# Performance work log

Hardware: AMD Instinct MI355X
Metric: run time of the kernel (lower is better)

Reference implementation:

```python
import jax, jax.numpy as jnp
import numpy as np

DIM = 128
EXPAND = 2
INTERNAL = DIM * EXPAND  # 256
MAX_SEQ = 2048
BATCH = 32
GATE_DECAY = 3.0


def _gated_cell(x, Wa, ba, Wi, bi, g):
    # x: [B,S,D]; Wa,Wi: [E,D]; ba,bi,g: [E]
    pa = jnp.einsum('bsd,ed->bse', x, Wa) + ba          # projected activation
    pi = jnp.einsum('bsd,ed->bse', x, Wi) + bi          # projected input
    reset_gate = jax.nn.sigmoid(pa)
    input_gate = jax.nn.sigmoid(pi)
    alpha = jax.nn.sigmoid(g)                           # [E]
    a = alpha / jnp.power(GATE_DECAY, reset_gate)       # adaptive alpha [B,S,E]
    u = jnp.sqrt(1.0 - a * a) * (input_gate * pi)       # per-step input [B,S,E]

    def step(h, au):
        a_t, u_t = au
        h = a_t * h + u_t
        return h, h

    h0 = jnp.zeros((x.shape[0], Wa.shape[0]), x.dtype)
    _, ys = jax.lax.scan(step, h0, (a.transpose(1, 0, 2), u.transpose(1, 0, 2)))
    return ys.transpose(1, 0, 2)                        # [B,S,E]


def _recency_weights(seq_len, dtype):
    w = jnp.exp(jnp.linspace(0.0, 3.0, MAX_SEQ))[:seq_len]
    return w.astype(dtype).reshape(1, -1, 1)


def setup_inputs() -> dict:
    key = jax.random.key(0)
    ks = jax.random.split(key, 12)
    std = 1.0 / np.sqrt(DIM)  # kaiming fan_in linear
    lo = float(np.log(0.9 / 0.1))
    hi = float(np.log(0.999 / 0.001))
    d = {
        'x': jax.random.normal(ks[0], (BATCH, MAX_SEQ, DIM), jnp.float32),
        'Wa_u': jax.random.normal(ks[1], (INTERNAL, DIM), jnp.float32) * std,
        'ba_u': jnp.zeros((INTERNAL,), jnp.float32),
        'Wi_u': jax.random.normal(ks[2], (INTERNAL, DIM), jnp.float32) * std,
        'bi_u': jnp.zeros((INTERNAL,), jnp.float32),
        'g_u': jax.random.uniform(ks[3], (INTERNAL,), jnp.float32, lo, hi),
        'Wa_w': jax.random.normal(ks[4], (INTERNAL, DIM), jnp.float32) * std,
        'ba_w': jnp.zeros((INTERNAL,), jnp.float32),
        'Wi_w': jax.random.normal(ks[5], (INTERNAL, DIM), jnp.float32) * std,
        'bi_w': jnp.zeros((INTERNAL,), jnp.float32),
        'g_w': jax.random.uniform(ks[6], (INTERNAL,), jnp.float32, lo, hi),
        'Wf': jax.random.normal(ks[7], (DIM, 4 * DIM), jnp.float32) * (1.0 / np.sqrt(4 * DIM)),
        'bf': jnp.zeros((DIM,), jnp.float32),
    }
    return d


def reference(x, Wa_u, ba_u, Wi_u, bi_u, g_u, Wa_w, ba_w, Wi_w, bi_w, g_w, Wf, bf):
    unweighted = _gated_cell(x, Wa_u, ba_u, Wi_u, bi_u, g_u)          # [B,S,2D]
    xw = x * _recency_weights(x.shape[1], x.dtype)
    weighted = _gated_cell(xw, Wa_w, ba_w, Wi_w, bi_w, g_w)           # [B,S,2D]
    combined = jnp.concatenate([unweighted, weighted], axis=-1)       # [B,S,4D]
    return jnp.einsum('bsf,df->bsd', combined, Wf) + bf               # [B,S,D]
```

## Files before the change

### kernel.cpp

```cpp
#include <hip/hip_runtime.h>
#include <hip/hip_fp16.h>
#include <cstddef>
#include <cstdint>

#define DIM 128
#define SEQ 2048
#define NB 32
#define NCH 512
#define NROWS (NB * SEQ)

typedef _Float16 half8 __attribute__((ext_vector_type(8)));
typedef float    f32x4 __attribute__((ext_vector_type(4)));

#define CMB_BYTES ((size_t)NROWS * NCH * 2)
#define WFG_OFF   CMB_BYTES
#define WFG_BYTES ((size_t)NCH * DIM * 2)
#define WS_NEEDED (WFG_OFF + WFG_BYTES)

__device__ __forceinline__ float sigf(float v) {
    return __builtin_amdgcn_rcpf(1.0f + __builtin_amdgcn_exp2f(v * -1.44269504f));
}

__device__ __forceinline__ half8 cvt8(float4 v0, float4 v1) {
    auto p0 = __builtin_amdgcn_cvt_pkrtz(v0.x, v0.y);
    auto p1 = __builtin_amdgcn_cvt_pkrtz(v0.z, v0.w);
    auto p2 = __builtin_amdgcn_cvt_pkrtz(v1.x, v1.y);
    auto p3 = __builtin_amdgcn_cvt_pkrtz(v1.z, v1.w);
    union U { half8 h8; decltype(p0) p[4]; } u;
    u.p[0] = p0; u.p[1] = p1; u.p[2] = p2; u.p[3] = p3;
    return u.h8;
}

__device__ __forceinline__ void gload_lds16(const _Float16* g, _Float16* l) {
    __builtin_amdgcn_global_load_lds(
        (const __attribute__((address_space(1))) void*)g,
        (__attribute__((address_space(3))) void*)l,
        16, 0, 0);
}

__global__ __launch_bounds__(512, 2) void kfused(
        const float* __restrict__ x,
        const float* __restrict__ Wa_u, const float* __restrict__ ba_u,
        const float* __restrict__ Wi_u, const float* __restrict__ bi_u,
        const float* __restrict__ g_u,
        const float* __restrict__ Wa_w, const float* __restrict__ ba_w,
        const float* __restrict__ Wi_w, const float* __restrict__ bi_w,
        const float* __restrict__ g_w,
        const float* __restrict__ Wf, _Float16* __restrict__ Wfg,
        _Float16* __restrict__ cmb) {
    __shared__ _Float16 Bs[8192];
    __shared__ float2   Wseg[2][8][33];
    __shared__ float    carryL[2][32];

    const int tid  = threadIdx.x;
    const int lane = tid & 63;
    const int w    = tid >> 6;
    const int quad = lane >> 4;
    const int n16  = lane & 15;

    const int b  = blockIdx.x;
    const int cg = blockIdx.y;
    const int p  = cg >> 3;
    const int ebase = (cg & 7) * 32;

    if (b == 0) {
        int tg = cg * 512 + tid;
#pragma unroll
        for (int i = 0; i < 8; ++i) {
            int o = tg * 8 + i;
            int j    = o & 7;
            int l2   = (o >> 3) & 63;
            int q2   = l2 >> 4, m16 = l2 & 15;
            int ct   = (o >> 9) & 7;
            int ks2  = (o >> 12) & 1;
            int kb2  = o >> 13;
            int k = kb2 * 64 + ks2 * 32 + q2 * 8 + j;
            int n = ct * 16 + m16;
            Wfg[o] = (_Float16)Wf[n * NCH + k];
        }
    }

    const float* Wa  = p ? Wa_w : Wa_u;
    const float* Wi  = p ? Wi_w : Wi_u;
    const float* bap = p ? ba_w : ba_u;
    const float* bip = p ? bi_w : bi_u;
    const float* gp  = p ? g_w  : g_u;

    for (int sl = tid; sl < 1024; sl += 512) {
        int l  = sl & 63;
        int nt = (sl >> 6) & 3;
        int ks = sl >> 8;
        int qq = l >> 4, nn = l & 15;
        int e = ebase + (nt & 1) * 16 + nn;
        const float* Wp = (nt >> 1) ? Wi : Wa;
        const float* src = Wp + (size_t)e * DIM + ks * 32 + qq * 8;
        float4 v0 = *(const float4*)src;
        float4 v1 = *(const float4*)(src + 4);
        *(half8*)&Bs[sl * 8] = cvt8(v0, v1);
    }

    const float NL2E = -1.44269504f;
    float rba[2], rbi[2], ral[2], rba2[2];
#pragma unroll
    for (int hh = 0; hh < 2; ++hh) {
        int e = ebase + hh * 16 + n16;
        rba[hh] = bap[e];
        rbi[hh] = bip[e];
        ral[hh] = sigf(gp[e]);
        rba2[hh] = rba[hh] * NL2E;
    }
    if (tid < 32) carryL[0][tid] = 0.0f;

    float scb = __expf((float)(w * 16 + quad * 4) * (3.0f / 2047.0f));
    const float r1    = __expf(3.0f / 2047.0f);
    const float r2    = r1 * r1;
    const float r3    = r2 * r1;
    const float cs128 = __expf(128.0f * 3.0f / 2047.0f);

    const float* xbase = x + ((size_t)b * SEQ + (size_t)(w * 16 + n16)) * DIM + quad * 8;
    _Float16* dst0 = cmb + (size_t)(cg >> 1) * 8192 + (size_t)w * 1024
                   + (size_t)(cg & 1) * 512
                   + (size_t)quad * 32 + (size_t)(n16 >> 3) * 128 + (n16 & 7);

    __syncthreads();

    half8 bfr[8];
#pragma unroll
    for (int ks = 0; ks < 2; ++ks)
#pragma unroll
        for (int nt = 0; nt < 4; ++nt)
            bfr[ks * 4 + nt] = *(const half8*)&Bs[(ks * 256 + nt * 64 + lane) * 8];

    half8 af[4];
    {
        float4 xf0[8];
#pragma unroll
        for (int ks = 0; ks < 4; ++ks) {
            xf0[2 * ks]     = *(const float4*)(xbase + ks * 32);
            xf0[2 * ks + 1] = *(const float4*)(xbase + ks * 32 + 4);
        }
#pragma unroll
        for (int ks = 0; ks < 4; ++ks)
            af[ks] = cvt8(xf0[2 * ks], xf0[2 * ks + 1]);
    }

    for (int t = 0; t < 16; ++t) {
        f32x4 acc[4];
#pragma unroll
        for (int nt = 0; nt < 4; ++nt) acc[nt] = (f32x4){0.f, 0.f, 0.f, 0.f};
#pragma unroll
        for (int ks = 0; ks < 4; ++ks) {
            half8 a = af[ks];
#pragma unroll
            for (int nt = 0; nt < 4; ++nt) {
                half8 bb = (ks < 2)
                    ? bfr[ks * 4 + nt]
                    : *(const half8*)&Bs[(ks * 256 + nt * 64 + lane) * 8];
                acc[nt] = __builtin_amdgcn_mfma_f32_16x16x32_f16(a, bb, acc[nt], 0, 0, 0);
            }
        }

        const float* ab = xbase + (size_t)((t + 1) & 15) * 128 * DIM;
        float4 xf1[4];
#pragma unroll
        for (int ks = 0; ks < 2; ++ks) {
            xf1[2 * ks]     = *(const float4*)(ab + ks * 32);
            xf1[2 * ks + 1] = *(const float4*)(ab + ks * 32 + 4);
        }

        float sc[4], sc2[4];
        if (p) { sc[0] = scb; sc[1] = scb * r1; sc[2] = scb * r2; sc[3] = scb * r3; }
        else   { sc[0] = sc[1] = sc[2] = sc[3] = 1.0f; }
        scb *= cs128;
#pragma unroll
        for (int reg = 0; reg < 4; ++reg) sc2[reg] = sc[reg] * NL2E;

        float a_s[2][4], u_s[2][4];
        float IA[2], IU[2], EA[2], EU[2];
#pragma unroll
        for (int hh = 0; hh < 2; ++hh) {
            float A4 = 1.0f, U4 = 0.0f;
#pragma unroll
            for (int reg = 0; reg < 4; ++reg) {
                float pi  = fmaf(acc[2 + hh][reg], sc[reg], rbi[hh]);
                float ea  = __builtin_amdgcn_exp2f(fmaf(acc[hh][reg], sc2[reg], rba2[hh]));
                float rst = __builtin_amdgcn_rcpf(1.0f + ea);
                float ig  = sigf(pi);
                float a   = ral[hh] * __builtin_amdgcn_exp2f(-rst * 1.5849625007211562f);
                float m   = fmaxf(fmaf(-a, a, 1.0f), 0.0f);
                float u   = __builtin_amdgcn_sqrtf(m) * (ig * pi);
                a_s[hh][reg] = a; u_s[hh][reg] = u;
                A4 *= a;
                U4 = fmaf(a, U4, u);
            }
            float A = A4, U = U4;
            float Ap = __shfl_up(A, 16); float Up = __shfl_up(U, 16);
            bool c1 = quad >= 1;
            U = c1 ? fmaf(A, Up, U) : U;
            A = c1 ? A * Ap : A;
            Ap = __shfl_up(A, 32); Up = __shfl_up(U, 32);
            bool c2 = quad >= 2;
            U = c2 ? fmaf(A, Up, U) : U;
            A = c2 ? A * Ap : A;
            IA[hh] = A; IU[hh] = U;
            float Ae = __shfl_up(A, 16), Ue = __shfl_up(U, 16);
            EA[hh] = (quad == 0) ? 1.0f : Ae;
            EU[hh] = (quad == 0) ? 0.0f : Ue;
        }
        if (quad == 3) {
#pragma unroll
            for (int hh = 0; hh < 2; ++hh)
                Wseg[t & 1][w][hh * 16 + n16] = make_float2(IA[hh], IU[hh]);
        }

        __syncthreads();

        float4 xf2[4];
#pragma unroll
        for (int ks = 0; ks < 2; ++ks) {
            xf2[2 * ks]     = *(const float4*)(ab + 64 + ks * 32);
            xf2[2 * ks + 1] = *(const float4*)(ab + 64 + ks * 32 + 4);
        }
        af[0] = cvt8(xf1[0], xf1[1]);
        af[1] = cvt8(xf1[2], xf1[3]);

        _Float16* dstT = dst0 + (size_t)((b * 16 + t) * 8) * 8192;
#pragma unroll
        for (int hh = 0; hh < 2; ++hh) {
            int ch = hh * 16 + n16;
            float h = carryL[t & 1][ch];
            float2 wv[7];
#pragma unroll
            for (int jj = 0; jj < 7; ++jj)
                wv[jj] = Wseg[t & 1][jj][ch];
#pragma unroll
            for (int jj = 0; jj < 7; ++jj)
                if (jj < w) h = fmaf(wv[jj].x, h, wv[jj].y);
            h = fmaf(EA[hh], h, EU[hh]);
#pragma unroll
            for (int reg = 0; reg < 4; ++reg) {
                h = fmaf(a_s[hh][reg], h, u_s[hh][reg]);
                dstT[hh * 256 + reg * 8] = (_Float16)h;
            }
            if (w == 7 && quad == 3)
                carryL[(t + 1) & 1][ch] = h;
        }

        af[2] = cvt8(xf2[0], xf2[1]);
        af[3] = cvt8(xf2[2], xf2[3]);
    }
}

__global__ __launch_bounds__(256, 4) void k3_mfma(
        const _Float16* __restrict__ cmbF, const _Float16* __restrict__ Wfg,
        const float* __restrict__ bfv, float* __restrict__ out) {
    __shared__ _Float16 As[2][4096];

    const int tid  = threadIdx.x;
    const int lane = tid & 63;
    const int w    = tid >> 6;
    const int id   = blockIdx.x;
    const int rb   = id >> 1;
    const int half = id & 1;
    const int rt7  = half * 4 + w;
    const int q    = lane >> 4;
    const int nn   = lane & 15;

    f32x4 acc[8];
#pragma unroll
    for (int ct = 0; ct < 8; ++ct) acc[ct] = (f32x4){0.0f, 0.0f, 0.0f, 0.0f};

#define K3_STAGE(buf, kb)                                                     \
    {                                                                         \
        const _Float16* sa = cmbF + ((size_t)rb * 8 + (kb)) * 8192            \
                           + (size_t)rt7 * 1024 + (size_t)lane * 8;           \
        _Float16* la = &As[buf][w * 1024];                                    \
        gload_lds16(sa, la);                                                  \
        gload_lds16(sa + 512, la + 512);                                      \
    }

    K3_STAGE(0, 0);
    __syncthreads();

    for (int kb = 0; kb < 8; ++kb) {
        const int cur = kb & 1;
        if (kb < 7) K3_STAGE(cur ^ 1, kb + 1);

        const _Float16* bsrc = Wfg + (size_t)kb * 8192 + (size_t)lane * 8;
#pragma unroll
        for (int ks = 0; ks < 2; ++ks) {
            half8 a = *(const half8*)&As[cur][w * 1024 + ks * 512 + lane * 8];
#pragma unroll
            for (int ct = 0; ct < 8; ++ct) {
                half8 bb = *(const half8*)(bsrc + (size_t)(ks * 8 + ct) * 512);
                acc[ct] = __builtin_amdgcn_mfma_f32_16x16x32_f16(a, bb, acc[ct], 0, 0, 0);
            }
        }
        __syncthreads();
    }

    const int rbase = rb * 128 + rt7 * 16 + q * 4;
#pragma unroll
    for (int ct = 0; ct < 8; ++ct) {
        int col = ct * 16 + nn;
        float bias = bfv[col];
#pragma unroll
        for (int reg = 0; reg < 4; ++reg)
            out[(size_t)(rbase + reg) * DIM + col] = acc[ct][reg] + bias;
    }
#undef K3_STAGE
}

extern "C" void kernel_launch(void* const* d_in, const int* in_sizes, int n_in,
                              void* d_out, int out_size, void* d_ws, size_t ws_size,
                              hipStream_t stream) {
    if (ws_size < WS_NEEDED) return;

    const float* x    = (const float*)d_in[0];
    const float* Wa_u = (const float*)d_in[1];
    const float* ba_u = (const float*)d_in[2];
    const float* Wi_u = (const float*)d_in[3];
    const float* bi_u = (const float*)d_in[4];
    const float* g_u  = (const float*)d_in[5];
    const float* Wa_w = (const float*)d_in[6];
    const float* ba_w = (const float*)d_in[7];
    const float* Wi_w = (const float*)d_in[8];
    const float* bi_w = (const float*)d_in[9];
    const float* g_w  = (const float*)d_in[10];
    const float* Wf   = (const float*)d_in[11];
    const float* bfv  = (const float*)d_in[12];
    float* out = (float*)d_out;

    char* ws = (char*)d_ws;
    _Float16* cmb = (_Float16*)ws;
    _Float16* Wfg = (_Float16*)(ws + WFG_OFF);

    hipLaunchKernelGGL(kfused, dim3(32, 16), dim3(512), 0, stream,
                       x, Wa_u, ba_u, Wi_u, bi_u, g_u,
                       Wa_w, ba_w, Wi_w, bi_w, g_w, Wf, Wfg, cmb);
    hipLaunchKernelGGL(k3_mfma, dim3(1024), dim3(256), 0, stream,
                       cmb, Wfg, bfv, out);
}
```

Baseline: 206.8 us.

## Stage Wf tiles in LDS with a three-buffer async pipeline in k3

The final projection kernel now also stages the Wf weight tiles into shared memory through async global-to-LDS loads, instead of reading them straight from global memory for every MFMA. The double buffer becomes a triple buffer with a prefetch depth of two, synchronised by explicit vmcnt waits and raw barriers in place of __syncthreads. This is meant to hide global load latency and cut repeated global traffic for the B operand. In exchange, LDS use rises to about 72 KB per block, so launch bounds drop to 2 blocks per CU, which may reduce occupancy.

```diff
diff --git a/kernel.cpp b/kernel.cpp
--- a/kernel.cpp
+++ b/kernel.cpp
@@ -251,10 +251,11 @@
     }
 }
 
-__global__ __launch_bounds__(256, 4) void k3_mfma(
+__global__ __launch_bounds__(256, 2) void k3_mfma(
         const _Float16* __restrict__ cmbF, const _Float16* __restrict__ Wfg,
         const float* __restrict__ bfv, float* __restrict__ out) {
-    __shared__ _Float16 As[2][4096];
+    __shared__ __align__(16) _Float16 As[3][4096];
+    __shared__ __align__(16) _Float16 Bs[3][8192];
 
     const int tid  = threadIdx.x;
     const int lane = tid & 63;
@@ -262,7 +263,6 @@
     const int id   = blockIdx.x;
     const int rb   = id >> 1;
     const int half = id & 1;
-    const int rt7  = half * 4 + w;
     const int q    = lane >> 4;
     const int nn   = lane & 15;
 
@@ -273,33 +273,44 @@
 #define K3_STAGE(buf, kb)                                                     \
     {                                                                         \
         const _Float16* sa = cmbF + ((size_t)rb * 8 + (kb)) * 8192            \
-                           + (size_t)rt7 * 1024 + (size_t)lane * 8;           \
+                           + (size_t)half * 4096 + (size_t)w * 1024           \
+                           + (size_t)lane * 8;                                \
         _Float16* la = &As[buf][w * 1024];                                    \
         gload_lds16(sa, la);                                                  \
         gload_lds16(sa + 512, la + 512);                                      \
+        const _Float16* sb = Wfg + (size_t)(kb) * 8192                        \
+                           + (size_t)w * 2048 + (size_t)lane * 8;             \
+        _Float16* lb = &Bs[buf][w * 2048];                                    \
+        _Pragma("unroll")                                                     \
+        for (int i = 0; i < 4; ++i)                                           \
+            gload_lds16(sb + i * 512, lb + i * 512);                          \
     }
 
     K3_STAGE(0, 0);
-    __syncthreads();
+    K3_STAGE(1, 1);
 
     for (int kb = 0; kb < 8; ++kb) {
-        const int cur = kb & 1;
-        if (kb < 7) K3_STAGE(cur ^ 1, kb + 1);
-
-        const _Float16* bsrc = Wfg + (size_t)kb * 8192 + (size_t)lane * 8;
+        const int cur = kb % 3;
+        if (kb < 7) asm volatile("s_waitcnt vmcnt(6)" ::: "memory");
+        else        asm volatile("s_waitcnt vmcnt(0)" ::: "memory");
+        __builtin_amdgcn_s_barrier();
+        __builtin_amdgcn_sched_barrier(0);
+
+        if (kb < 6) K3_STAGE((kb + 2) % 3, kb + 2);
+
 #pragma unroll
         for (int ks = 0; ks < 2; ++ks) {
             half8 a = *(const half8*)&As[cur][w * 1024 + ks * 512 + lane * 8];
 #pragma unroll
             for (int ct = 0; ct < 8; ++ct) {
-                half8 bb = *(const half8*)(bsrc + (size_t)(ks * 8 + ct) * 512);
+                half8 bb = *(const half8*)&Bs[cur][(ks * 8 + ct) * 512 + lane * 8];
                 acc[ct] = __builtin_amdgcn_mfma_f32_16x16x32_f16(a, bb, acc[ct], 0, 0, 0);
             }
         }
-        __syncthreads();
-    }
-
-    const int rbase = rb * 128 + rt7 * 16 + q * 4;
+        __builtin_amdgcn_sched_barrier(0);
+    }
+
+    const int rbase = rb * 128 + half * 64 + w * 16 + q * 4;
 #pragma unroll
     for (int ct = 0; ct < 8; ++ct) {
         int col = ct * 16 + nn;
```

After: 191.5 us. 7.4% less time.
